# Performance work log

Hardware: AMD Instinct MI355X
Metric: run time of the kernel (lower is better)

## Reference

```python
import jax, jax.numpy as jnp
import numpy as np

D_MODEL = 1024
N_HEADS = 16
HEAD_DIM = D_MODEL // N_HEADS


def setup_inputs() -> dict:
    key = jax.random.key(0)
    ks = jax.random.split(key, 9)
    s = 1.0 / np.sqrt(D_MODEL)
    x = jax.random.normal(ks[0], (2, 2048, D_MODEL), dtype=jnp.float32)
    Wq = jax.random.uniform(ks[1], (D_MODEL, D_MODEL), jnp.float32, -s, s)
    bq = jax.random.uniform(ks[2], (D_MODEL,), jnp.float32, -s, s)
    Wk = jax.random.uniform(ks[3], (D_MODEL, D_MODEL), jnp.float32, -s, s)
    bk = jax.random.uniform(ks[4], (D_MODEL,), jnp.float32, -s, s)
    Wv = jax.random.uniform(ks[5], (D_MODEL, D_MODEL), jnp.float32, -s, s)
    bv = jax.random.uniform(ks[6], (D_MODEL,), jnp.float32, -s, s)
    Wo = jax.random.uniform(ks[7], (D_MODEL, D_MODEL), jnp.float32, -s, s)
    bo = jax.random.uniform(ks[8], (D_MODEL,), jnp.float32, -s, s)
    return {"x": x, "Wq": Wq, "bq": bq, "Wk": Wk, "bk": bk,
            "Wv": Wv, "bv": bv, "Wo": Wo, "bo": bo}


def reference(x, Wq, bq, Wk, bk, Wv, bv, Wo, bo):
    B, S, _ = x.shape
    # project and split heads: [B, H, S, Dh]
    def heads(W, b):
        return (x @ W + b).reshape(B, S, N_HEADS, HEAD_DIM).transpose(0, 2, 1, 3)
    Q, K, V = heads(Wq, bq), heads(Wk, bk), heads(Wv, bv)
    scale = 1.0 / np.sqrt(HEAD_DIM).astype(np.float32)
    scores = jnp.einsum('bhsd,bhtd->bhst', Q, K) * scale  # [B,H,S,S]
    causal = jnp.tril(jnp.ones((S, S), dtype=bool))
    scores = jnp.where(causal, scores, -jnp.inf)
    attn = jax.nn.softmax(scores, axis=-1)
    out = jnp.einsum('bhst,bhtd->bhsd', attn, V)  # [B,H,S,Dh]
    out = out.transpose(0, 2, 1, 3).reshape(B, S, D_MODEL)
    return out @ Wo + bo
```

## Files before the change

### kernel.cpp

```cpp
#include <hip/hip_runtime.h>

typedef __attribute__((ext_vector_type(8))) __bf16 bfrag;
typedef __attribute__((ext_vector_type(4))) float f32x4;

#define MFMA(a, b, c) __builtin_amdgcn_mfma_f32_16x16x32_bf16((a), (b), (c), 0, 0, 0)

#define D_MODEL 1024
#define SEQ     2048
#define NB      2
#define NH      16
#define HD      64
#define MROWS   (NB * SEQ)

#define SCALE_LOG2 0.18033688011112043f
#define NEG_BIG    (-3.0e38f)

#define GLOBAL_AS(p) ((const __attribute__((address_space(1))) void*)(p))
#define LDS_AS(p)    ((__attribute__((address_space(3))) void*)(p))
#define ASYNC_CP16(g, l) __builtin_amdgcn_global_load_lds(GLOBAL_AS(g), LDS_AS(l), 16, 0, 0)

__global__ __launch_bounds__(256) void k_prep(
    const float* __restrict__ x,
    const float* __restrict__ Wq, const float* __restrict__ Wk,
    const float* __restrict__ Wv, const float* __restrict__ Wo,
    __bf16* __restrict__ Wt, __bf16* __restrict__ xb)
{
    __shared__ __bf16 t[64][65];
    if (blockIdx.z == 4) {
        size_t base = ((size_t)(blockIdx.y * 16 + blockIdx.x)) * 16384;
        for (int j = 0; j < 8; ++j) {
            size_t i = base + (size_t)j * 2048 + (size_t)threadIdx.x * 8;
            float4 f0 = *(const float4*)&x[i];
            float4 f1 = *(const float4*)&x[i + 4];
            union { uint4 u; __bf16 h[8]; } cv;
            cv.h[0] = (__bf16)f0.x; cv.h[1] = (__bf16)f0.y;
            cv.h[2] = (__bf16)f0.z; cv.h[3] = (__bf16)f0.w;
            cv.h[4] = (__bf16)f1.x; cv.h[5] = (__bf16)f1.y;
            cv.h[6] = (__bf16)f1.z; cv.h[7] = (__bf16)f1.w;
            *(uint4*)&xb[i] = cv.u;
        }
        return;
    }
    const float* src = (blockIdx.z == 0) ? Wq : (blockIdx.z == 1) ? Wk
                      : (blockIdx.z == 2) ? Wv : Wo;
    __bf16* dst = Wt + (size_t)blockIdx.z * (1024u * 1024u);
    int tr = blockIdx.y * 64, tc = blockIdx.x * 64;
    for (int j = 0; j < 4; ++j) {
        int id = threadIdx.x + j * 256;
        int r = id >> 4;
        int c4 = (id & 15) * 4;
        float4 f = *(const float4*)&src[(size_t)(tr + r) * 1024 + tc + c4];
        t[r][c4 + 0] = (__bf16)f.x; t[r][c4 + 1] = (__bf16)f.y;
        t[r][c4 + 2] = (__bf16)f.z; t[r][c4 + 3] = (__bf16)f.w;
    }
    __syncthreads();
    for (int j = 0; j < 2; ++j) {
        int id = threadIdx.x + j * 256;
        int r = id >> 3;
        int c8 = (id & 7) * 8;
        union { uint4 u; __bf16 h[8]; } pk;
        for (int i = 0; i < 8; ++i) pk.h[i] = t[c8 + i][r];
        *(uint4*)&dst[(size_t)(tc + r) * 1024 + tr + c8] = pk.u;
    }
}

template <int MODE, bool WT>
__global__ __launch_bounds__(256) void k_gemm128(
    const void* __restrict__ Ap,
    const void* __restrict__ W0, const void* __restrict__ W1,
    const void* __restrict__ W2,
    const float* __restrict__ b0, const float* __restrict__ b1,
    const float* __restrict__ b2, void* __restrict__ dstp)
{
    constexpr int AST = WT ? 64 : 72;
    alignas(16) __shared__ __bf16 SH[18432];
    __bf16* As = SH;
    __bf16* Bs = SH + 128 * AST;

    const int tid = threadIdx.x;
    const int z = blockIdx.z;
    const int lid = blockIdx.x + (blockIdx.y << 3);
    const int mt = ((lid & 7) << 2) + ((lid >> 3) >> 3);
    const int nt = (lid >> 3) & 7;
    const int m0 = mt * 128;
    const int n0 = nt * 128;
    const void* W     = (z == 0) ? W0 : (z == 1) ? W1 : W2;
    const float* bias = (z == 0) ? b0 : (z == 1) ? b1 : b2;

    const int wid = tid >> 6, lane = tid & 63;
    const int quad = lane >> 4, l16 = lane & 15;
    const int wRow = (wid >> 1) * 64, wCol = (wid & 1) * 64;

    f32x4 acc[4][4];
    const f32x4 zero = {0.f, 0.f, 0.f, 0.f};
    for (int mi = 0; mi < 4; ++mi)
        for (int ni = 0; ni < 4; ++ni) acc[mi][ni] = zero;

    const int srow = tid >> 3;
    const int sseg = (tid & 7) * 8;
    const int bkrow = tid >> 4;
    const int bnseg = (tid & 15) * 8;
    const int arow = lane >> 3;
    const int akoff = ((lane & 7) * 8) ^ (arow * 8);
    const int sw = (l16 & 7) * 8;

    for (int k0 = 0; k0 < D_MODEL; k0 += 64) {
        __syncthreads();
        if (WT) {
            const __bf16* Ab = (const __bf16*)Ap;
            const __bf16* Bt = (const __bf16*)W;
            for (int it = 0; it < 4; ++it) {
                int row = wid * 32 + it * 8;
                ASYNC_CP16(&Ab[(size_t)(m0 + row + arow) * D_MODEL + k0 + akoff],
                           &As[row * 64]);
                ASYNC_CP16(&Bt[(size_t)(n0 + row + arow) * D_MODEL + k0 + akoff],
                           &Bs[row * 64]);
            }
        } else {
            if (MODE == 0) {
                const float* A = (const float*)Ap;
                for (int it = 0; it < 4; ++it) {
                    int row = srow + it * 32;
                    const float* src = &A[(size_t)(m0 + row) * D_MODEL + k0 + sseg];
                    float4 f0 = *(const float4*)src;
                    float4 f1 = *(const float4*)(src + 4);
                    union { uint4 u; __bf16 h[8]; } cv;
                    cv.h[0] = (__bf16)f0.x; cv.h[1] = (__bf16)f0.y;
                    cv.h[2] = (__bf16)f0.z; cv.h[3] = (__bf16)f0.w;
                    cv.h[4] = (__bf16)f1.x; cv.h[5] = (__bf16)f1.y;
                    cv.h[6] = (__bf16)f1.z; cv.h[7] = (__bf16)f1.w;
                    *(uint4*)&As[row * AST + sseg] = cv.u;
                }
            } else {
                const __bf16* A = (const __bf16*)Ap;
                for (int it = 0; it < 4; ++it) {
                    int row = srow + it * 32;
                    uint4 va = *(const uint4*)&A[(size_t)(m0 + row) * D_MODEL + k0 + sseg];
                    *(uint4*)&As[row * AST + sseg] = va;
                }
            }
            const float* Wf = (const float*)W;
            for (int it = 0; it < 4; ++it) {
                int krow = bkrow + it * 16;
                const float* src = &Wf[(size_t)(k0 + krow) * D_MODEL + n0 + bnseg];
                float4 f0 = *(const float4*)src;
                float4 f1 = *(const float4*)(src + 4);
                Bs[(bnseg + 0) * AST + krow] = (__bf16)f0.x;
                Bs[(bnseg + 1) * AST + krow] = (__bf16)f0.y;
                Bs[(bnseg + 2) * AST + krow] = (__bf16)f0.z;
                Bs[(bnseg + 3) * AST + krow] = (__bf16)f0.w;
                Bs[(bnseg + 4) * AST + krow] = (__bf16)f1.x;
                Bs[(bnseg + 5) * AST + krow] = (__bf16)f1.y;
                Bs[(bnseg + 6) * AST + krow] = (__bf16)f1.z;
                Bs[(bnseg + 7) * AST + krow] = (__bf16)f1.w;
            }
        }
        __syncthreads();
        for (int kk = 0; kk < 64; kk += 32) {
            bfrag af[4], bf[4];
            if (WT) {
                int ko = (kk + quad * 8) ^ sw;
                for (int mi = 0; mi < 4; ++mi)
                    af[mi] = *(const bfrag*)&As[(wRow + mi * 16 + l16) * 64 + ko];
                for (int ni = 0; ni < 4; ++ni)
                    bf[ni] = *(const bfrag*)&Bs[(wCol + ni * 16 + l16) * 64 + ko];
            } else {
                for (int mi = 0; mi < 4; ++mi)
                    af[mi] = *(const bfrag*)&As[(wRow + mi * 16 + l16) * AST + kk + quad * 8];
                for (int ni = 0; ni < 4; ++ni)
                    bf[ni] = *(const bfrag*)&Bs[(wCol + ni * 16 + l16) * AST + kk + quad * 8];
            }
            for (int mi = 0; mi < 4; ++mi)
                for (int ni = 0; ni < 4; ++ni)
                    acc[mi][ni] = MFMA(af[mi], bf[ni], acc[mi][ni]);
        }
    }

    if (MODE == 0) {
        float biasv[4];
        for (int ni = 0; ni < 4; ++ni) biasv[ni] = bias[n0 + wCol + ni * 16 + l16];
        const int b = m0 >> 11, m0s = m0 & 2047, h0 = n0 >> 6;
        __syncthreads();
        if (z < 2) {
            for (int mi = 0; mi < 4; ++mi)
                for (int ni = 0; ni < 4; ++ni) {
                    int col = wCol + ni * 16 + l16;
                    for (int r = 0; r < 4; ++r) {
                        float v = acc[mi][ni][r] + biasv[ni];
                        if (z == 0) v *= SCALE_LOG2;
                        SH[(wRow + mi * 16 + quad * 4 + r) * 136 + col] = (__bf16)v;
                    }
                }
            __syncthreads();
            __bf16* qk = (__bf16*)dstp + (size_t)z * (MROWS * (size_t)D_MODEL);
            for (int i = 0; i < 8; ++i) {
                int rid = i * 32 + (tid >> 3);
                int hl = rid >> 7, sl = rid & 127;
                int dcol = (tid & 7) * 8;
                uint4 v = *(const uint4*)&SH[sl * 136 + hl * 64 + dcol];
                *(uint4*)&qk[(((size_t)b * NH + h0 + hl) * SEQ + m0s + sl) * HD + dcol] = v;
            }
        } else {
            for (int mi = 0; mi < 4; ++mi)
                for (int ni = 0; ni < 4; ++ni) {
                    int col = wCol + ni * 16 + l16;
                    int s0 = wRow + mi * 16 + quad * 4;
                    union { unsigned long long u; __bf16 h4[4]; } pk;
                    for (int r = 0; r < 4; ++r)
                        pk.h4[r] = (__bf16)(acc[mi][ni][r] + biasv[ni]);
                    *(unsigned long long*)&SH[col * 136 + s0] = pk.u;
                }
            __syncthreads();
            __bf16* vv = (__bf16*)dstp + (size_t)2 * (MROWS * (size_t)D_MODEL);
            for (int i = 0; i < 8; ++i) {
                int rid = i * 16 + (tid >> 4);
                int hl = rid >> 6, d = rid & 63;
                int sc = (tid & 15) * 8;
                uint4 v = *(const uint4*)&SH[rid * 136 + sc];
                *(uint4*)&vv[(((size_t)b * NH + h0 + hl) * HD + d) * SEQ + m0s + sc] = v;
            }
        }
    } else {
        for (int mi = 0; mi < 4; ++mi)
            for (int ni = 0; ni < 4; ++ni) {
                int gn = n0 + wCol + ni * 16 + l16;
                float bv = bias[gn];
                for (int r = 0; r < 4; ++r) {
                    int gm = m0 + wRow + mi * 16 + quad * 4 + r;
                    ((float*)dstp)[(size_t)gm * D_MODEL + gn] = acc[mi][ni][r] + bv;
                }
            }
    }
}

__global__ __launch_bounds__(256) void k_gemm_out(
    const __bf16* __restrict__ A, const __bf16* __restrict__ Bt,
    const float* __restrict__ bias, float* __restrict__ dst)
{
    alignas(16) __shared__ __bf16 As[64 * 64];
    alignas(16) __shared__ __bf16 Bs[128 * 64];

    const int tid = threadIdx.x;
    const int lid = blockIdx.x + (blockIdx.y << 3);
    const int mt = ((lid & 7) << 3) + ((lid >> 3) >> 3);
    const int nt = (lid >> 3) & 7;
    const int m0 = mt * 64;
    const int n0 = nt * 128;
    const int wid = tid >> 6, lane = tid & 63;
    const int quad = lane >> 4, l16 = lane & 15;
    const int wRow = (wid >> 1) * 32, wCol = (wid & 1) * 64;

    f32x4 acc[2][4];
    const f32x4 zero = {0.f, 0.f, 0.f, 0.f};
    for (int mi = 0; mi < 2; ++mi)
        for (int ni = 0; ni < 4; ++ni) acc[mi][ni] = zero;

    const int arow = lane >> 3;
    const int akoff = ((lane & 7) * 8) ^ (arow * 8);
    const int sw = (l16 & 7) * 8;

    for (int k0 = 0; k0 < D_MODEL; k0 += 64) {
        __syncthreads();
        for (int it = 0; it < 2; ++it) {
            int row = wid * 16 + it * 8;
            ASYNC_CP16(&A[(size_t)(m0 + row + arow) * D_MODEL + k0 + akoff],
                       &As[row * 64]);
        }
        for (int it = 0; it < 4; ++it) {
            int row = wid * 32 + it * 8;
            ASYNC_CP16(&Bt[(size_t)(n0 + row + arow) * D_MODEL + k0 + akoff],
                       &Bs[row * 64]);
        }
        __syncthreads();
        for (int kk = 0; kk < 64; kk += 32) {
            int ko = (kk + quad * 8) ^ sw;
            bfrag af[2], bf[4];
            for (int mi = 0; mi < 2; ++mi)
                af[mi] = *(const bfrag*)&As[(wRow + mi * 16 + l16) * 64 + ko];
            for (int ni = 0; ni < 4; ++ni)
                bf[ni] = *(const bfrag*)&Bs[(wCol + ni * 16 + l16) * 64 + ko];
            for (int mi = 0; mi < 2; ++mi)
                for (int ni = 0; ni < 4; ++ni)
                    acc[mi][ni] = MFMA(af[mi], bf[ni], acc[mi][ni]);
        }
    }

    for (int mi = 0; mi < 2; ++mi)
        for (int ni = 0; ni < 4; ++ni) {
            int gn = n0 + wCol + ni * 16 + l16;
            float bv = bias[gn];
            for (int r = 0; r < 4; ++r) {
                int gm = m0 + wRow + mi * 16 + quad * 4 + r;
                dst[(size_t)gm * D_MODEL + gn] = acc[mi][ni][r] + bv;
            }
        }
}

__global__ __launch_bounds__(256) void k_attn(
    const __bf16* __restrict__ Q, const __bf16* __restrict__ K,
    const __bf16* __restrict__ Vt, __bf16* __restrict__ O)
{
    alignas(16) __shared__ __bf16 Ks[64 * 64];
    alignas(16) __shared__ __bf16 Vts[64 * 64];
    alignas(16) __shared__ __bf16 Ps[4][16 * 64];

    const int tid = threadIdx.x, wid = tid >> 6, lane = tid & 63;
    const int quad = lane >> 4, l16 = lane & 15;
    const int u = (blockIdx.x + blockIdx.y + blockIdx.z) & 15;
    const int h = blockIdx.y, b = blockIdx.z;
    const size_t bh = ((size_t)b * NH + h) * SEQ * HD;
    const __bf16* Kg  = K + bh;
    const __bf16* Vtg = Vt + ((size_t)b * NH + h) * HD * SEQ;

    union { uint4 u; bfrag f; } onesu;
    onesu.u = make_uint4(0x3F803F80u, 0x3F803F80u, 0x3F803F80u, 0x3F803F80u);
    const bfrag onesf = onesu.f;

    const f32x4 zero = {0.f, 0.f, 0.f, 0.f};
    const int sw = (l16 & 7) * 8;
    const int row0 = tid >> 3, seg = (tid & 7) * 8;
    const int sseg = seg ^ ((row0 & 7) * 8);

    const __bf16* Kr0 = &Kg[(size_t)row0 * HD + seg];
    const __bf16* Kr1 = &Kg[(size_t)(row0 + 32) * HD + seg];
    const __bf16* Vr0 = &Vtg[(size_t)row0 * SEQ + seg];
    const __bf16* Vr1 = &Vtg[(size_t)(row0 + 32) * SEQ + seg];

    for (int pass = 0; pass < 2; ++pass) {
        const int qb = pass ? u : (31 - u);
        const __bf16* Qg = Q + bh + (size_t)qb * 64 * HD;

        bfrag qf0 = *(const bfrag*)&Qg[(size_t)(wid * 16 + l16) * HD + quad * 8];
        bfrag qf1 = *(const bfrag*)&Qg[(size_t)(wid * 16 + l16) * HD + 32 + quad * 8];

        f32x4 o[4];
        for (int dt = 0; dt < 4; ++dt) o[dt] = zero;
        f32x4 o_l = zero;
        const int q = qb * 64 + wid * 16 + l16;
        const int ntile = qb + 1;

        uint4 kreg0 = *(const uint4*)(Kr0);
        uint4 kreg1 = *(const uint4*)(Kr1);
        uint4 vreg0 = *(const uint4*)(Vr0);
        uint4 vreg1 = *(const uint4*)(Vr1);

        for (int t = 0; t < ntile; ++t) {
            const int j0 = t * 64;
            __syncthreads();
            *(uint4*)&Ks[row0 * 64 + sseg] = kreg0;
            *(uint4*)&Ks[(row0 + 32) * 64 + sseg] = kreg1;
            *(uint4*)&Vts[row0 * 64 + sseg] = vreg0;
            *(uint4*)&Vts[(row0 + 32) * 64 + sseg] = vreg1;
            if (t + 1 < ntile) {
                const size_t j1k = (size_t)(j0 + 64) * HD;
                const int j1v = j0 + 64;
                kreg0 = *(const uint4*)(Kr0 + j1k);
                kreg1 = *(const uint4*)(Kr1 + j1k);
                vreg0 = *(const uint4*)(Vr0 + j1v);
                vreg1 = *(const uint4*)(Vr1 + j1v);
            }
            __syncthreads();

            f32x4 st[4];
            for (int kt = 0; kt < 4; ++kt) {
                bfrag ka0 = *(const bfrag*)&Ks[(kt * 16 + l16) * 64 + ((quad * 8) ^ sw)];
                bfrag ka1 = *(const bfrag*)&Ks[(kt * 16 + l16) * 64 + ((32 + quad * 8) ^ sw)];
                st[kt] = MFMA(ka1, qf1, MFMA(ka0, qf0, zero));
            }

            if (t == ntile - 1) {
                for (int kt = 0; kt < 4; ++kt)
                    for (int r = 0; r < 4; ++r) {
                        float v = (j0 + kt * 16 + quad * 4 + r > q) ? NEG_BIG : st[kt][r];
                        st[kt][r] = exp2f(v);
                    }
            } else {
                for (int kt = 0; kt < 4; ++kt)
                    for (int r = 0; r < 4; ++r)
                        st[kt][r] = exp2f(st[kt][r]);
            }

            for (int kt = 0; kt < 4; ++kt) {
                union { unsigned long long u; __bf16 h4[4]; } pk;
                for (int r = 0; r < 4; ++r) pk.h4[r] = (__bf16)st[kt][r];
                *(unsigned long long*)&Ps[wid][l16 * 64 + ((kt * 16 + quad * 4) ^ sw)] = pk.u;
            }
            asm volatile("s_waitcnt lgkmcnt(0)" ::: "memory");

            for (int c = 0; c < 2; ++c) {
                int ko = (c * 32 + quad * 8) ^ sw;
                bfrag pf = *(const bfrag*)&Ps[wid][l16 * 64 + ko];
                for (int dt = 0; dt < 4; ++dt) {
                    bfrag vf = *(const bfrag*)&Vts[(dt * 16 + l16) * 64 + ko];
                    o[dt] = MFMA(pf, vf, o[dt]);
                }
                o_l = MFMA(pf, onesf, o_l);
            }
        }

        for (int r = 0; r < 4; ++r) {
            float inv = 1.0f / o_l[r];
            size_t base = ((size_t)b * SEQ + qb * 64 + wid * 16 + quad * 4 + r) * D_MODEL
                        + (size_t)h * HD;
            for (int dt = 0; dt < 4; ++dt)
                O[base + dt * 16 + l16] = (__bf16)(o[dt][r] * inv);
        }
    }
}

extern "C" void kernel_launch(void* const* d_in, const int* in_sizes, int n_in,
                              void* d_out, int out_size, void* d_ws, size_t ws_size,
                              hipStream_t stream)
{
    const float* x  = (const float*)d_in[0];
    const float* Wq = (const float*)d_in[1];
    const float* bq = (const float*)d_in[2];
    const float* Wk = (const float*)d_in[3];
    const float* bk = (const float*)d_in[4];
    const float* Wv = (const float*)d_in[5];
    const float* bv = (const float*)d_in[6];
    const float* Wo = (const float*)d_in[7];
    const float* bo = (const float*)d_in[8];

    __bf16* ws = (__bf16*)d_ws;
    const size_t M1 = 1024u * 1024u;
    __bf16* qkv    = ws;
    __bf16* attn_o = ws + 12 * M1;
    __bf16* Wt     = ws + 16 * M1;
    __bf16* xb     = ws + 20 * M1;

    const bool fast = ws_size >= (size_t)48 * 1024 * 1024;

    if (fast) {
        k_prep<<<dim3(16, 16, 5), 256, 0, stream>>>(x, Wq, Wk, Wv, Wo, Wt, xb);
        k_gemm128<0, true><<<dim3(8, 32, 3), 256, 0, stream>>>(
            xb, Wt, Wt + M1, Wt + 2 * M1, bq, bk, bv, qkv);
        k_attn<<<dim3(16, 16, 2), 256, 0, stream>>>(
            qkv, qkv + 4 * M1, qkv + 8 * M1, attn_o);
        k_gemm_out<<<dim3(8, 64), 256, 0, stream>>>(
            attn_o, Wt + 3 * M1, bo, (float*)d_out);
    } else {
        k_gemm128<0, false><<<dim3(8, 32, 3), 256, 0, stream>>>(
            x, Wq, Wk, Wv, bq, bk, bv, qkv);
        k_attn<<<dim3(16, 16, 2), 256, 0, stream>>>(
            qkv, qkv + 4 * M1, qkv + 8 * M1, attn_o);
        k_gemm128<1, false><<<dim3(8, 32, 1), 256, 0, stream>>>(
            attn_o, Wo, Wo, Wo, bo, bo, bo, (float*)d_out);
    }
}
```

Baseline: 188.8 us.

## Merge two causal query-block passes into one K/V sweep sharing LDS tiles

```diff
diff --git a/kernel.cpp b/kernel.cpp
--- a/kernel.cpp
+++ b/kernel.cpp
@@ -308,16 +308,31 @@
     const int quad = lane >> 4, l16 = lane & 15;
     const int u = (blockIdx.x + blockIdx.y + blockIdx.z) & 15;
     const int h = blockIdx.y, b = blockIdx.z;
+    const int qbA = 31 - u, qbB = u;
     const size_t bh = ((size_t)b * NH + h) * SEQ * HD;
     const __bf16* Kg  = K + bh;
     const __bf16* Vtg = Vt + ((size_t)b * NH + h) * HD * SEQ;
 
+    const __bf16* QgA = Q + bh + (size_t)qbA * 64 * HD;
+    const __bf16* QgB = Q + bh + (size_t)qbB * 64 * HD;
+    bfrag qfA0 = *(const bfrag*)&QgA[(size_t)(wid * 16 + l16) * HD + quad * 8];
+    bfrag qfA1 = *(const bfrag*)&QgA[(size_t)(wid * 16 + l16) * HD + 32 + quad * 8];
+    bfrag qfB0 = *(const bfrag*)&QgB[(size_t)(wid * 16 + l16) * HD + quad * 8];
+    bfrag qfB1 = *(const bfrag*)&QgB[(size_t)(wid * 16 + l16) * HD + 32 + quad * 8];
+
     union { uint4 u; bfrag f; } onesu;
     onesu.u = make_uint4(0x3F803F80u, 0x3F803F80u, 0x3F803F80u, 0x3F803F80u);
     const bfrag onesf = onesu.f;
 
     const f32x4 zero = {0.f, 0.f, 0.f, 0.f};
+    f32x4 oA[4], oB[4];
+    for (int dt = 0; dt < 4; ++dt) { oA[dt] = zero; oB[dt] = zero; }
+    f32x4 o_lA = zero, o_lB = zero;
+    const int qA = qbA * 64 + wid * 16 + l16;
+    const int qB = qbB * 64 + wid * 16 + l16;
+    const int ntA = qbA + 1, ntB = qbB + 1;
     const int sw = (l16 & 7) * 8;
+
     const int row0 = tid >> 3, seg = (tid & 7) * 8;
     const int sseg = seg ^ ((row0 & 7) * 8);
 
@@ -326,52 +341,40 @@
     const __bf16* Vr0 = &Vtg[(size_t)row0 * SEQ + seg];
     const __bf16* Vr1 = &Vtg[(size_t)(row0 + 32) * SEQ + seg];
 
-    for (int pass = 0; pass < 2; ++pass) {
-        const int qb = pass ? u : (31 - u);
-        const __bf16* Qg = Q + bh + (size_t)qb * 64 * HD;
-
-        bfrag qf0 = *(const bfrag*)&Qg[(size_t)(wid * 16 + l16) * HD + quad * 8];
-        bfrag qf1 = *(const bfrag*)&Qg[(size_t)(wid * 16 + l16) * HD + 32 + quad * 8];
-
-        f32x4 o[4];
-        for (int dt = 0; dt < 4; ++dt) o[dt] = zero;
-        f32x4 o_l = zero;
-        const int q = qb * 64 + wid * 16 + l16;
-        const int ntile = qb + 1;
-
-        uint4 kreg0 = *(const uint4*)(Kr0);
-        uint4 kreg1 = *(const uint4*)(Kr1);
-        uint4 vreg0 = *(const uint4*)(Vr0);
-        uint4 vreg1 = *(const uint4*)(Vr1);
-
-        for (int t = 0; t < ntile; ++t) {
-            const int j0 = t * 64;
-            __syncthreads();
-            *(uint4*)&Ks[row0 * 64 + sseg] = kreg0;
-            *(uint4*)&Ks[(row0 + 32) * 64 + sseg] = kreg1;
-            *(uint4*)&Vts[row0 * 64 + sseg] = vreg0;
-            *(uint4*)&Vts[(row0 + 32) * 64 + sseg] = vreg1;
-            if (t + 1 < ntile) {
-                const size_t j1k = (size_t)(j0 + 64) * HD;
-                const int j1v = j0 + 64;
-                kreg0 = *(const uint4*)(Kr0 + j1k);
-                kreg1 = *(const uint4*)(Kr1 + j1k);
-                vreg0 = *(const uint4*)(Vr0 + j1v);
-                vreg1 = *(const uint4*)(Vr1 + j1v);
-            }
-            __syncthreads();
-
+    uint4 kreg0 = *(const uint4*)(Kr0);
+    uint4 kreg1 = *(const uint4*)(Kr1);
+    uint4 vreg0 = *(const uint4*)(Vr0);
+    uint4 vreg1 = *(const uint4*)(Vr1);
+
+    for (int t = 0; t < ntA; ++t) {
+        const int j0 = t * 64;
+        __syncthreads();
+        *(uint4*)&Ks[row0 * 64 + sseg] = kreg0;
+        *(uint4*)&Ks[(row0 + 32) * 64 + sseg] = kreg1;
+        *(uint4*)&Vts[row0 * 64 + sseg] = vreg0;
+        *(uint4*)&Vts[(row0 + 32) * 64 + sseg] = vreg1;
+        if (t + 1 < ntA) {
+            const size_t j1k = (size_t)(j0 + 64) * HD;
+            const int j1v = j0 + 64;
+            kreg0 = *(const uint4*)(Kr0 + j1k);
+            kreg1 = *(const uint4*)(Kr1 + j1k);
+            vreg0 = *(const uint4*)(Vr0 + j1v);
+            vreg1 = *(const uint4*)(Vr1 + j1v);
+        }
+        __syncthreads();
+
+        {
             f32x4 st[4];
             for (int kt = 0; kt < 4; ++kt) {
                 bfrag ka0 = *(const bfrag*)&Ks[(kt * 16 + l16) * 64 + ((quad * 8) ^ sw)];
                 bfrag ka1 = *(const bfrag*)&Ks[(kt * 16 + l16) * 64 + ((32 + quad * 8) ^ sw)];
-                st[kt] = MFMA(ka1, qf1, MFMA(ka0, qf0, zero));
-            }
-
-            if (t == ntile - 1) {
+                st[kt] = MFMA(ka1, qfA1, MFMA(ka0, qfA0, zero));
+            }
+
+            if (t == ntA - 1) {
                 for (int kt = 0; kt < 4; ++kt)
                     for (int r = 0; r < 4; ++r) {
-                        float v = (j0 + kt * 16 + quad * 4 + r > q) ? NEG_BIG : st[kt][r];
+                        float v = (j0 + kt * 16 + quad * 4 + r > qA) ? NEG_BIG : st[kt][r];
                         st[kt][r] = exp2f(v);
                     }
             } else {
@@ -392,19 +395,64 @@
                 bfrag pf = *(const bfrag*)&Ps[wid][l16 * 64 + ko];
                 for (int dt = 0; dt < 4; ++dt) {
                     bfrag vf = *(const bfrag*)&Vts[(dt * 16 + l16) * 64 + ko];
-                    o[dt] = MFMA(pf, vf, o[dt]);
-                }
-                o_l = MFMA(pf, onesf, o_l);
-            }
-        }
-
-        for (int r = 0; r < 4; ++r) {
-            float inv = 1.0f / o_l[r];
-            size_t base = ((size_t)b * SEQ + qb * 64 + wid * 16 + quad * 4 + r) * D_MODEL
-                        + (size_t)h * HD;
-            for (int dt = 0; dt < 4; ++dt)
-                O[base + dt * 16 + l16] = (__bf16)(o[dt][r] * inv);
-        }
+                    oA[dt] = MFMA(pf, vf, oA[dt]);
+                }
+                o_lA = MFMA(pf, onesf, o_lA);
+            }
+        }
+
+        if (t < ntB) {
+            f32x4 st[4];
+            for (int kt = 0; kt < 4; ++kt) {
+                bfrag ka0 = *(const bfrag*)&Ks[(kt * 16 + l16) * 64 + ((quad * 8) ^ sw)];
+                bfrag ka1 = *(const bfrag*)&Ks[(kt * 16 + l16) * 64 + ((32 + quad * 8) ^ sw)];
+                st[kt] = MFMA(ka1, qfB1, MFMA(ka0, qfB0, zero));
+            }
+
+            if (t == ntB - 1) {
+                for (int kt = 0; kt < 4; ++kt)
+                    for (int r = 0; r < 4; ++r) {
+                        float v = (j0 + kt * 16 + quad * 4 + r > qB) ? NEG_BIG : st[kt][r];
+                        st[kt][r] = exp2f(v);
+                    }
+            } else {
+                for (int kt = 0; kt < 4; ++kt)
+                    for (int r = 0; r < 4; ++r)
+                        st[kt][r] = exp2f(st[kt][r]);
+            }
+
+            for (int kt = 0; kt < 4; ++kt) {
+                union { unsigned long long u; __bf16 h4[4]; } pk;
+                for (int r = 0; r < 4; ++r) pk.h4[r] = (__bf16)st[kt][r];
+                *(unsigned long long*)&Ps[wid][l16 * 64 + ((kt * 16 + quad * 4) ^ sw)] = pk.u;
+            }
+            asm volatile("s_waitcnt lgkmcnt(0)" ::: "memory");
+
+            for (int c = 0; c < 2; ++c) {
+                int ko = (c * 32 + quad * 8) ^ sw;
+                bfrag pf = *(const bfrag*)&Ps[wid][l16 * 64 + ko];
+                for (int dt = 0; dt < 4; ++dt) {
+                    bfrag vf = *(const bfrag*)&Vts[(dt * 16 + l16) * 64 + ko];
+                    oB[dt] = MFMA(pf, vf, oB[dt]);
+                }
+                o_lB = MFMA(pf, onesf, o_lB);
+            }
+        }
+    }
+
+    for (int r = 0; r < 4; ++r) {
+        float inv = 1.0f / o_lA[r];
+        size_t base = ((size_t)b * SEQ + qbA * 64 + wid * 16 + quad * 4 + r) * D_MODEL
+                    + (size_t)h * HD;
+        for (int dt = 0; dt < 4; ++dt)
+            O[base + dt * 16 + l16] = (__bf16)(oA[dt][r] * inv);
+    }
+    for (int r = 0; r < 4; ++r) {
+        float inv = 1.0f / o_lB[r];
+        size_t base = ((size_t)b * SEQ + qbB * 64 + wid * 16 + quad * 4 + r) * D_MODEL
+                    + (size_t)h * HD;
+        for (int dt = 0; dt < 4; ++dt)
+            O[base + dt * 16 + l16] = (__bf16)(oB[dt][r] * inv);
     }
 }
 
```

New measurement: 189.6 us. About the same (+0.4%).

## Process both causal query blocks concurrently in one 512-thread attention block

Applied to the files above, without the earlier changes.

```diff
diff --git a/kernel.cpp b/kernel.cpp
--- a/kernel.cpp
+++ b/kernel.cpp
@@ -296,79 +296,75 @@
         }
 }
 
-__global__ __launch_bounds__(256) void k_attn(
+__global__ __launch_bounds__(512) void k_attn(
     const __bf16* __restrict__ Q, const __bf16* __restrict__ K,
     const __bf16* __restrict__ Vt, __bf16* __restrict__ O)
 {
     alignas(16) __shared__ __bf16 Ks[64 * 64];
     alignas(16) __shared__ __bf16 Vts[64 * 64];
-    alignas(16) __shared__ __bf16 Ps[4][16 * 64];
-
-    const int tid = threadIdx.x, wid = tid >> 6, lane = tid & 63;
+    alignas(16) __shared__ __bf16 Ps[8][16 * 64];
+
+    const int tid = threadIdx.x;
+    const int wid8 = tid >> 6;
+    const int grp = wid8 >> 2;
+    const int wid = wid8 & 3;
+    const int lane = tid & 63;
     const int quad = lane >> 4, l16 = lane & 15;
     const int u = (blockIdx.x + blockIdx.y + blockIdx.z) & 15;
     const int h = blockIdx.y, b = blockIdx.z;
+    const int qb = grp ? u : (31 - u);
+    const int ntA = 32 - u;
+    const int nt  = qb + 1;
     const size_t bh = ((size_t)b * NH + h) * SEQ * HD;
     const __bf16* Kg  = K + bh;
     const __bf16* Vtg = Vt + ((size_t)b * NH + h) * HD * SEQ;
 
+    const __bf16* Qg = Q + bh + (size_t)qb * 64 * HD;
+    bfrag qf0 = *(const bfrag*)&Qg[(size_t)(wid * 16 + l16) * HD + quad * 8];
+    bfrag qf1 = *(const bfrag*)&Qg[(size_t)(wid * 16 + l16) * HD + 32 + quad * 8];
+
     union { uint4 u; bfrag f; } onesu;
     onesu.u = make_uint4(0x3F803F80u, 0x3F803F80u, 0x3F803F80u, 0x3F803F80u);
     const bfrag onesf = onesu.f;
 
     const f32x4 zero = {0.f, 0.f, 0.f, 0.f};
+    f32x4 o[4];
+    for (int dt = 0; dt < 4; ++dt) o[dt] = zero;
+    f32x4 o_l = zero;
+    const int q = qb * 64 + wid * 16 + l16;
     const int sw = (l16 & 7) * 8;
-    const int row0 = tid >> 3, seg = (tid & 7) * 8;
+
+    const int row0 = tid >> 3;
+    const int seg = (tid & 7) * 8;
     const int sseg = seg ^ ((row0 & 7) * 8);
 
-    const __bf16* Kr0 = &Kg[(size_t)row0 * HD + seg];
-    const __bf16* Kr1 = &Kg[(size_t)(row0 + 32) * HD + seg];
-    const __bf16* Vr0 = &Vtg[(size_t)row0 * SEQ + seg];
-    const __bf16* Vr1 = &Vtg[(size_t)(row0 + 32) * SEQ + seg];
-
-    for (int pass = 0; pass < 2; ++pass) {
-        const int qb = pass ? u : (31 - u);
-        const __bf16* Qg = Q + bh + (size_t)qb * 64 * HD;
-
-        bfrag qf0 = *(const bfrag*)&Qg[(size_t)(wid * 16 + l16) * HD + quad * 8];
-        bfrag qf1 = *(const bfrag*)&Qg[(size_t)(wid * 16 + l16) * HD + 32 + quad * 8];
-
-        f32x4 o[4];
-        for (int dt = 0; dt < 4; ++dt) o[dt] = zero;
-        f32x4 o_l = zero;
-        const int q = qb * 64 + wid * 16 + l16;
-        const int ntile = qb + 1;
-
-        uint4 kreg0 = *(const uint4*)(Kr0);
-        uint4 kreg1 = *(const uint4*)(Kr1);
-        uint4 vreg0 = *(const uint4*)(Vr0);
-        uint4 vreg1 = *(const uint4*)(Vr1);
-
-        for (int t = 0; t < ntile; ++t) {
-            const int j0 = t * 64;
-            __syncthreads();
-            *(uint4*)&Ks[row0 * 64 + sseg] = kreg0;
-            *(uint4*)&Ks[(row0 + 32) * 64 + sseg] = kreg1;
-            *(uint4*)&Vts[row0 * 64 + sseg] = vreg0;
-            *(uint4*)&Vts[(row0 + 32) * 64 + sseg] = vreg1;
-            if (t + 1 < ntile) {
-                const size_t j1k = (size_t)(j0 + 64) * HD;
-                const int j1v = j0 + 64;
-                kreg0 = *(const uint4*)(Kr0 + j1k);
-                kreg1 = *(const uint4*)(Kr1 + j1k);
-                vreg0 = *(const uint4*)(Vr0 + j1v);
-                vreg1 = *(const uint4*)(Vr1 + j1v);
-            }
-            __syncthreads();
-
+    const __bf16* Kr = &Kg[(size_t)row0 * HD + seg];
+    const __bf16* Vr = &Vtg[(size_t)row0 * SEQ + seg];
+    uint4 kreg = *(const uint4*)(Kr);
+    uint4 vreg = *(const uint4*)(Vr);
+
+    for (int t = 0; t < ntA; ++t) {
+        const int j0 = t * 64;
+        __syncthreads();
+        *(uint4*)&Ks[row0 * 64 + sseg] = kreg;
+        *(uint4*)&Vts[row0 * 64 + sseg] = vreg;
+        if (t + 1 < ntA) {
+            kreg = *(const uint4*)(Kr + (size_t)(j0 + 64) * HD);
+            vreg = *(const uint4*)(Vr + j0 + 64);
+        }
+        __syncthreads();
+
+        if (t < nt) {
             f32x4 st[4];
+            __builtin_amdgcn_s_setprio(1);
             for (int kt = 0; kt < 4; ++kt) {
                 bfrag ka0 = *(const bfrag*)&Ks[(kt * 16 + l16) * 64 + ((quad * 8) ^ sw)];
                 bfrag ka1 = *(const bfrag*)&Ks[(kt * 16 + l16) * 64 + ((32 + quad * 8) ^ sw)];
                 st[kt] = MFMA(ka1, qf1, MFMA(ka0, qf0, zero));
             }
-
-            if (t == ntile - 1) {
+            __builtin_amdgcn_s_setprio(0);
+
+            if (t == nt - 1) {
                 for (int kt = 0; kt < 4; ++kt)
                     for (int r = 0; r < 4; ++r) {
                         float v = (j0 + kt * 16 + quad * 4 + r > q) ? NEG_BIG : st[kt][r];
@@ -383,28 +379,30 @@
             for (int kt = 0; kt < 4; ++kt) {
                 union { unsigned long long u; __bf16 h4[4]; } pk;
                 for (int r = 0; r < 4; ++r) pk.h4[r] = (__bf16)st[kt][r];
-                *(unsigned long long*)&Ps[wid][l16 * 64 + ((kt * 16 + quad * 4) ^ sw)] = pk.u;
+                *(unsigned long long*)&Ps[wid8][l16 * 64 + ((kt * 16 + quad * 4) ^ sw)] = pk.u;
             }
             asm volatile("s_waitcnt lgkmcnt(0)" ::: "memory");
 
+            __builtin_amdgcn_s_setprio(1);
             for (int c = 0; c < 2; ++c) {
                 int ko = (c * 32 + quad * 8) ^ sw;
-                bfrag pf = *(const bfrag*)&Ps[wid][l16 * 64 + ko];
+                bfrag pf = *(const bfrag*)&Ps[wid8][l16 * 64 + ko];
                 for (int dt = 0; dt < 4; ++dt) {
                     bfrag vf = *(const bfrag*)&Vts[(dt * 16 + l16) * 64 + ko];
                     o[dt] = MFMA(pf, vf, o[dt]);
                 }
                 o_l = MFMA(pf, onesf, o_l);
             }
-        }
-
-        for (int r = 0; r < 4; ++r) {
-            float inv = 1.0f / o_l[r];
-            size_t base = ((size_t)b * SEQ + qb * 64 + wid * 16 + quad * 4 + r) * D_MODEL
-                        + (size_t)h * HD;
-            for (int dt = 0; dt < 4; ++dt)
-                O[base + dt * 16 + l16] = (__bf16)(o[dt][r] * inv);
-        }
+            __builtin_amdgcn_s_setprio(0);
+        }
+    }
+
+    for (int r = 0; r < 4; ++r) {
+        float inv = 1.0f / o_l[r];
+        size_t base = ((size_t)b * SEQ + qb * 64 + wid * 16 + quad * 4 + r) * D_MODEL
+                    + (size_t)h * HD;
+        for (int dt = 0; dt < 4; ++dt)
+            O[base + dt * 16 + l16] = (__bf16)(o[dt][r] * inv);
     }
 }
 
@@ -435,14 +433,14 @@
         k_prep<<<dim3(16, 16, 5), 256, 0, stream>>>(x, Wq, Wk, Wv, Wo, Wt, xb);
         k_gemm128<0, true><<<dim3(8, 32, 3), 256, 0, stream>>>(
             xb, Wt, Wt + M1, Wt + 2 * M1, bq, bk, bv, qkv);
-        k_attn<<<dim3(16, 16, 2), 256, 0, stream>>>(
+        k_attn<<<dim3(16, 16, 2), 512, 0, stream>>>(
             qkv, qkv + 4 * M1, qkv + 8 * M1, attn_o);
         k_gemm_out<<<dim3(8, 64), 256, 0, stream>>>(
             attn_o, Wt + 3 * M1, bo, (float*)d_out);
     } else {
         k_gemm128<0, false><<<dim3(8, 32, 3), 256, 0, stream>>>(
             x, Wq, Wk, Wv, bq, bk, bv, qkv);
-        k_attn<<<dim3(16, 16, 2), 256, 0, stream>>>(
+        k_attn<<<dim3(16, 16, 2), 512, 0, stream>>>(
             qkv, qkv + 4 * M1, qkv + 8 * M1, attn_o);
         k_gemm128<1, false><<<dim3(8, 32, 1), 256, 0, stream>>>(
             attn_o, Wo, Wo, Wo, bo, bo, bo, (float*)d_out);
```

Measured after the change: 183.0 us. 3.1% less time.
